# Optimization experiments

Measured on AMD Instinct MI355X. Metric: run time of the kernel, lower is better.

## Reference

```python
import jax, jax.numpy as jnp
import numpy as np

HEADS = 16
DIMS = [64, 64, 64, 64]  # [d_att(Q), d_att(K), d_ff(V), d_ff(G)]
EPS = 1e-4
P_POW = 2


def _cdist(Q, K):
    # Euclidean pairwise distance via the norm expansion, like torch.cdist.
    # Q: [h, b, t, d], K: [h, b, t, d] -> [h, b, t, t]
    q2 = jnp.sum(Q * Q, axis=-1)  # [h, b, t]
    k2 = jnp.sum(K * K, axis=-1)  # [h, b, t]
    qk = jnp.einsum('hbtd,hbsd->hbts', Q, K)
    d2 = q2[..., :, None] + k2[..., None, :] - 2.0 * qk
    return jnp.sqrt(jnp.maximum(d2, 0.0))


def setup_inputs() -> dict:
    key = jax.random.key(0)
    ks = jax.random.split(key, 4)
    b, t, d_in = 2, 2048, 1024
    d_proj = HEADS * sum(DIMS)  # 4096
    X = jax.random.normal(ks[0], (b, t, d_in), dtype=jnp.float32)
    W_in = jax.random.normal(ks[1], (d_in, d_proj), dtype=jnp.float32) * (d_in ** -0.5)
    b_in = jnp.zeros((d_proj,), dtype=jnp.float32)
    W_out = jax.random.normal(ks[2], (HEADS * DIMS[2], d_in), dtype=jnp.float32) * ((HEADS * DIMS[2]) ** -0.5)
    b_out = jnp.zeros((d_in,), dtype=jnp.float32)
    return {"X": X, "W_in": W_in, "b_in": b_in, "W_out": W_out, "b_out": b_out}


def reference(X, W_in, b_in, W_out, b_out):
    b, t, _ = X.shape
    # multi-head input projection: [b,t,d_in] -> [h,b,t,sum(DIMS)] -> split
    P = X @ W_in + b_in                       # [b, t, h*sum(DIMS)]
    P = P.reshape(b, t, HEADS, sum(DIMS))
    P = jnp.transpose(P, (2, 0, 1, 3))        # [h, b, t, sum(DIMS)]
    splits = np.cumsum(DIMS)[:-1]
    Q, K, V, G = jnp.split(P, splits, axis=-1)
    # Shepard's attention: inverse-power-distance weights
    W = jnp.power(EPS + _cdist(Q, K), -P_POW)         # [h, b, t, t]
    W = W / (EPS + jnp.sum(W, axis=-1, keepdims=True))
    A = jnp.einsum('hbts,hbse->hbte', W, V)           # [h, b, t, e]
    H = G * A                                          # gating
    H = jnp.transpose(H, (1, 2, 0, 3)).reshape(b, t, HEADS * DIMS[2])
    return H @ W_out + b_out
```

## Files before the change

kernel.cpp:

```cpp
#include <hip/hip_runtime.h>
#include <hip/hip_bf16.h>
#include <cstdint>
#include <cstddef>

typedef __bf16 bf16_t;
typedef __attribute__((ext_vector_type(8))) __bf16 bf16x8;
typedef __attribute__((ext_vector_type(4))) float f32x4;
typedef __attribute__((ext_vector_type(16))) float f32x16;
typedef __attribute__((ext_vector_type(4))) unsigned int u32x4;

#define ATT_EPS 1e-4f

__device__ __forceinline__ f32x4 mfma_bf16(bf16x8 a, bf16x8 b, f32x4 c) {
  return __builtin_amdgcn_mfma_f32_16x16x32_bf16(a, b, c, 0, 0, 0);
}
__device__ __forceinline__ f32x16 mfma32(bf16x8 a, bf16x8 b, f32x16 c) {
  return __builtin_amdgcn_mfma_f32_32x32x16_bf16(a, b, c, 0, 0, 0);
}
__device__ __forceinline__ unsigned cvtpk_bf16(float lo, float hi) {
  unsigned r;
  asm("v_cvt_pk_bf16_f32 %0, %1, %2" : "=v"(r) : "v"(lo), "v"(hi));
  return r;
}

#define GLDS16(g, l)                                                          \
  __builtin_amdgcn_global_load_lds(                                           \
      (const __attribute__((address_space(1))) void*)(g),                     \
      (__attribute__((address_space(3))) void*)(l), 16, 0, 0)

__global__ __launch_bounds__(256) void cvt_x_kernel(
    const float* __restrict__ X, bf16_t* __restrict__ Xb, int n8) {
  int i = blockIdx.x * 256 + threadIdx.x;
  if (i >= n8) return;
  f32x4 a = ((const f32x4*)X)[i * 2 + 0];
  f32x4 b = ((const f32x4*)X)[i * 2 + 1];
  bf16x8 o;
  o[0] = (__bf16)a[0]; o[1] = (__bf16)a[1]; o[2] = (__bf16)a[2]; o[3] = (__bf16)a[3];
  o[4] = (__bf16)b[0]; o[5] = (__bf16)b[1]; o[6] = (__bf16)b[2]; o[7] = (__bf16)b[3];
  ((bf16x8*)Xb)[i] = o;
}

__global__ __launch_bounds__(256) void tcvt2_kernel(
    const float* __restrict__ Wi, bf16_t* __restrict__ WiT,
    const float* __restrict__ Wo, bf16_t* __restrict__ WoT) {
  __shared__ float T[64][65];
  int tx = threadIdx.x & 63, ty = threadIdx.x >> 6;
  const float* W;
  bf16_t* Wt;
  int c0, r0, R, C;
  if (blockIdx.y < 16) {
    W = Wi; Wt = WiT; R = 1024; C = 4096;
    c0 = blockIdx.x * 64; r0 = blockIdx.y * 64;
  } else {
    int idx = (blockIdx.y - 16) * 64 + blockIdx.x;
    if (idx >= 256) return;
    W = Wo; Wt = WoT; R = 1024; C = 1024;
    c0 = (idx & 15) * 64; r0 = (idx >> 4) * 64;
  }
#pragma unroll
  for (int i = 0; i < 16; ++i) {
    int rr = ty * 16 + i;
    T[rr][tx] = W[(size_t)(r0 + rr) * C + c0 + tx];
  }
  __syncthreads();
#pragma unroll
  for (int i = 0; i < 16; ++i) {
    int cc = ty * 16 + i;
    Wt[(size_t)(c0 + cc) * R + r0 + tx] = (bf16_t)T[tx][cc];
  }
}

template <int OUTF32, int FUSE>
__global__ __launch_bounds__(256, 2) void gemm_kernel(
    const bf16_t* __restrict__ A, const bf16_t* __restrict__ Bt,
    const float* __restrict__ bias, void* __restrict__ Cout,
    int M, int N, int K,
    float* __restrict__ Q2, bf16_t* __restrict__ K2E, bf16_t* __restrict__ VtG) {
  __shared__ bf16_t As[2][128 * 64];
  __shared__ bf16_t Bs[2][128 * 64];
  int tid = threadIdx.x, lane = tid & 63, wv = tid >> 6;
  int l15 = lane & 15, lhi = lane >> 4;
  int NT = N >> 7;
  int nwg = gridDim.x;
  int qq = nwg >> 3;
  int swz = (blockIdx.x & 7) * qq + (blockIdx.x >> 3);
  int tm = swz / NT, tn = swz % NT;
  int m0 = tm << 7, n0 = tn << 7;
  int wm = (wv >> 1) << 6, wn = (wv & 1) << 6;
  int KT = K >> 6;

  auto stage = [&](int buf, int kt) {
    int k0 = kt << 6;
#pragma unroll
    for (int s = 0; s < 4; ++s) {
      int t = s * 256 + tid;
      int row = t >> 3, u = t & 7;
      int cc = (u ^ (row & 7)) << 3;
      GLDS16(A + (size_t)(m0 + row) * K + k0 + cc, &As[buf][t * 8]);
    }
#pragma unroll
    for (int s = 0; s < 4; ++s) {
      int t = s * 256 + tid;
      int row = t >> 3, u = t & 7;
      int cc = (u ^ (row & 7)) << 3;
      GLDS16(Bt + (size_t)(n0 + row) * K + k0 + cc, &Bs[buf][t * 8]);
    }
  };

  f32x4 zero = {0.f, 0.f, 0.f, 0.f};
  f32x4 acc[4][4];
#pragma unroll
  for (int ms = 0; ms < 4; ++ms)
#pragma unroll
    for (int ns = 0; ns < 4; ++ns) acc[ms][ns] = zero;

  stage(0, 0);
  __syncthreads();
  int cur = 0;
  for (int kt = 0; kt < KT; ++kt) {
    if (kt + 1 < KT) stage(cur ^ 1, kt + 1);
#pragma unroll
    for (int ks = 0; ks < 2; ++ks) {
      bf16x8 af[4], bfr[4];
#pragma unroll
      for (int ms = 0; ms < 4; ++ms) {
        int row = wm + ms * 16 + l15;
        af[ms] = *(const bf16x8*)&As[cur][row * 64 + (((ks * 4 + lhi) ^ (row & 7)) << 3)];
      }
#pragma unroll
      for (int ns = 0; ns < 4; ++ns) {
        int col = wn + ns * 16 + l15;
        bfr[ns] = *(const bf16x8*)&Bs[cur][col * 64 + (((ks * 4 + lhi) ^ (col & 7)) << 3)];
      }
#pragma unroll
      for (int ms = 0; ms < 4; ++ms)
#pragma unroll
        for (int ns = 0; ns < 4; ++ns)
          acc[ms][ns] = mfma_bf16(af[ms], bfr[ns], acc[ms][ns]);
    }
    __syncthreads();
    cur ^= 1;
  }

#pragma unroll
  for (int ns = 0; ns < 4; ++ns) {
    float bv = bias[n0 + wn + ns * 16 + l15];
#pragma unroll
    for (int ms = 0; ms < 4; ++ms)
#pragma unroll
      for (int r = 0; r < 4; ++r) acc[ms][ns][r] += bv;
  }

  bool vg = FUSE && ((n0 >> 7) & 1);
  bool skipC = vg && (wn == 0);

  if (!skipC) {
#pragma unroll
    for (int ns = 0; ns < 4; ++ns) {
      int col = n0 + wn + ns * 16 + l15;
#pragma unroll
      for (int ms = 0; ms < 4; ++ms) {
        int rowb = m0 + wm + ms * 16 + lhi * 4;
#pragma unroll
        for (int r = 0; r < 4; ++r) {
          float v = acc[ms][ns][r];
          if (OUTF32)
            ((float*)Cout)[(size_t)(rowb + r) * N + col] = v;
          else
            ((bf16_t*)Cout)[(size_t)(rowb + r) * N + col] = (bf16_t)v;
        }
      }
    }
  }

  if (FUSE) {
    int h = n0 >> 8;
    if (!vg) {
#pragma unroll
      for (int ms = 0; ms < 4; ++ms)
#pragma unroll
        for (int r = 0; r < 4; ++r) {
          float s = 0.f;
#pragma unroll
          for (int ns = 0; ns < 4; ++ns) s += acc[ms][ns][r] * acc[ms][ns][r];
          s += __shfl_xor(s, 1);
          s += __shfl_xor(s, 2);
          s += __shfl_xor(s, 4);
          s += __shfl_xor(s, 8);
          if (l15 == 0) {
            int row = m0 + wm + ms * 16 + lhi * 4 + r;
            if (wn == 0) {
              Q2[h * 4096 + row] = s;
            } else {
              __bf16 kh = (__bf16)s;
              __bf16 kl = (__bf16)(s - (float)kh);
              bf16x8 rw;
              rw[0] = kh; rw[1] = kl;
              rw[2] = (__bf16)1.f; rw[3] = (__bf16)1.f;
              rw[4] = (__bf16)0.f; rw[5] = (__bf16)0.f;
              rw[6] = (__bf16)0.f; rw[7] = (__bf16)0.f;
              *(bf16x8*)&K2E[((size_t)h * 4096 + row) * 8] = rw;
            }
          }
        }
    } else {
      bf16_t* T = (bf16_t*)&As[0][0];
      if (wn == 0) {
#pragma unroll
        for (int ms = 0; ms < 4; ++ms)
#pragma unroll
          for (int ns = 0; ns < 4; ++ns)
#pragma unroll
            for (int r = 0; r < 4; ++r) {
              int row = wm + ms * 16 + lhi * 4 + r;
              int e = ns * 16 + l15;
              int prow = (row & ~15) | ((row & 3) | ((row & 4) << 1) | ((row & 8) >> 1));
              T[e * 136 + prow] = (bf16_t)acc[ms][ns][r];
            }
      }
      __syncthreads();
      int e = tid >> 2, c0 = (tid & 3) * 32;
      bf16_t* dst = VtG + (size_t)(h * 64 + e) * 4096 + m0 + c0;
#pragma unroll
      for (int j = 0; j < 4; ++j)
        *(bf16x8*)&dst[j * 8] = *(bf16x8*)&T[e * 136 + c0 + j * 8];
    }
  }
}

__global__ __launch_bounds__(512, 4) void attn_kernel(
    const bf16_t* __restrict__ P, const bf16_t* __restrict__ VtG,
    const float* __restrict__ Q2, const bf16_t* __restrict__ K2E,
    bf16_t* __restrict__ H) {
  __shared__ union Smem {
    struct {
      bf16_t Ks[2][64 * 64];
      bf16_t Vts[2][64 * 64];
      bf16_t K2e[2][64 * 8];
    } l;
    float Comb[4][64][33];
  } sm;
  __shared__ float invLds[4][32];

  int tid = threadIdx.x, lane = tid & 63, wv = tid >> 6;
  int l31 = lane & 31, hi = lane >> 5, hi4 = hi * 4;
  int qw = wv & 3, sw = wv >> 2;
  int sOff = sw * 32;
  int swz = (blockIdx.x & 7) * 64 + (blockIdx.x >> 3);
  int hb = swz >> 4, qt = swz & 15;
  int h = hb >> 1, b = hb & 1;
  int rowbase = b * 2048;
  const bf16_t* Pq = P + (size_t)rowbase * 4096 + h * 256;
  const bf16_t* Pk = Pq + 64;
  const bf16_t* Pg = Pq + 192;
  const bf16_t* Vg = VtG + (size_t)h * 64 * 4096 + rowbase;
  const float* Q2g = Q2 + h * 4096 + rowbase;
  const bf16_t* K2Eg = K2E + ((size_t)h * 4096 + rowbase) * 8;
  int q0 = qt * 128 + qw * 32;

  auto stageKV = [&](int buf, int s0) {
    {
      int row = tid >> 3, u = tid & 7;
      int cc = (u ^ (row & 7)) << 3;
      GLDS16(Pk + (size_t)(s0 + row) * 4096 + cc, &sm.l.Ks[buf][tid * 8]);
    }
    {
      int row = tid >> 3, u = tid & 7;
      int cc = (u ^ (row & 7)) << 3;
      GLDS16(Vg + (size_t)row * 4096 + s0 + cc, &sm.l.Vts[buf][tid * 8]);
    }
    if (tid < 64)
      GLDS16(K2Eg + (size_t)(s0 + tid) * 8, &sm.l.K2e[buf][tid * 8]);
  };

  bf16x8 qm[4];
#pragma unroll
  for (int db = 0; db < 4; ++db) {
    bf16x8 q = *(const bf16x8*)(Pq + (size_t)(q0 + l31) * 4096 + db * 16 + hi * 8);
    u32x4 u = *(u32x4*)&q;
    u = (u ^ 0x80008000u) + 0x00800080u;
    qm[db] = *(bf16x8*)&u;
  }
  float q2s = Q2g[q0 + l31];
  __bf16 q2h = (__bf16)q2s;
  __bf16 q2l = (__bf16)(q2s - (float)q2h);
  bf16x8 qmE;
  qmE[0] = hi ? (__bf16)0.f : (__bf16)1.f;
  qmE[1] = qmE[0];
  qmE[2] = hi ? (__bf16)0.f : q2h;
  qmE[3] = hi ? (__bf16)0.f : q2l;
  qmE[4] = (__bf16)0.f; qmE[5] = (__bf16)0.f;
  qmE[6] = (__bf16)0.f; qmE[7] = (__bf16)0.f;

  f32x16 zero16;
#pragma unroll
  for (int r = 0; r < 16; ++r) zero16[r] = 0.f;

  f32x16 nacc0 = zero16, nacc1 = zero16;
  float dacc0 = 0.f, dacc1 = 0.f;

  stageKV(0, 0);
  __syncthreads();

  for (int st = 0; st < 32; ++st) {
    int cur = st & 1;
    int s0 = st * 64;
    if (st + 1 < 32) stageKV(cur ^ 1, s0 + 64);

    const bf16_t* KsC = sm.l.Ks[cur];
    const bf16_t* VtC = sm.l.Vts[cur];
    const bf16_t* K2eC = sm.l.K2e[cur];
    {
      int srow = sOff + l31;
      bf16x8 ke = *(const bf16x8*)&K2eC[srow * 8];
      u32x4 keu = *(u32x4*)&ke;
      u32x4 kz;
      kz[0] = hi ? 0u : keu[0];
      kz[1] = hi ? 0u : keu[1];
      kz[2] = 0u; kz[3] = 0u;
      bf16x8 kfE = *(bf16x8*)&kz;
      f32x16 D = mfma32(kfE, qmE, zero16);
#pragma unroll
      for (int db = 0; db < 4; ++db) {
        bf16x8 kf = *(const bf16x8*)&KsC[srow * 64 + (((db * 2 + hi) ^ (srow & 7)) << 3)];
        D = mfma32(kf, qm[db], D);
      }
      float p[16];
#pragma unroll
      for (int r = 0; r < 16; ++r) {
        float w = __builtin_amdgcn_rcpf(fmaxf(D[r], 1e-12f));
        if (r & 1) dacc1 += w; else dacc0 += w;
        p[r] = w;
      }
      u32x4 w0v = {cvtpk_bf16(p[0], p[1]), cvtpk_bf16(p[2], p[3]),
                   cvtpk_bf16(p[4], p[5]), cvtpk_bf16(p[6], p[7])};
      u32x4 w1v = {cvtpk_bf16(p[8], p[9]), cvtpk_bf16(p[10], p[11]),
                   cvtpk_bf16(p[12], p[13]), cvtpk_bf16(p[14], p[15])};
      bf16x8 pa0 = *(bf16x8*)&w0v;
      bf16x8 pa1 = *(bf16x8*)&w1v;
      int e = l31;
      int ciB = sw * 4;
      bf16x8 vb00 = *(const bf16x8*)&VtC[e * 64 + (((ciB + 0 + hi) ^ (e & 7)) << 3)];
      bf16x8 vb01 = *(const bf16x8*)&VtC[(e + 32) * 64 + (((ciB + 0 + hi) ^ ((e + 32) & 7)) << 3)];
      bf16x8 vb10 = *(const bf16x8*)&VtC[e * 64 + (((ciB + 2 + hi) ^ (e & 7)) << 3)];
      bf16x8 vb11 = *(const bf16x8*)&VtC[(e + 32) * 64 + (((ciB + 2 + hi) ^ ((e + 32) & 7)) << 3)];
      nacc0 = mfma32(pa0, vb00, nacc0);
      nacc1 = mfma32(pa0, vb01, nacc1);
      nacc0 = mfma32(pa1, vb10, nacc0);
      nacc1 = mfma32(pa1, vb11, nacc1);
    }
    __syncthreads();
  }

  if (sw == 1) {
#pragma unroll
    for (int r = 0; r < 16; ++r) {
      sm.Comb[qw][lane][r] = nacc0[r];
      sm.Comb[qw][lane][16 + r] = nacc1[r];
    }
    sm.Comb[qw][lane][32] = dacc0 + dacc1;
  }
  __syncthreads();
  if (sw == 0) {
    float dacc = dacc0 + dacc1 + sm.Comb[qw][lane][32];
#pragma unroll
    for (int r = 0; r < 16; ++r) {
      nacc0[r] += sm.Comb[qw][lane][r];
      nacc1[r] += sm.Comb[qw][lane][16 + r];
    }
    dacc += __shfl_xor(dacc, 32);
    float inv = __builtin_amdgcn_rcpf(ATT_EPS + dacc);
    if (lane < 32) invLds[qw][l31] = inv;
    __builtin_amdgcn_s_waitcnt(0);
#pragma unroll
    for (int r = 0; r < 16; ++r) {
      int q = (r & 3) + 8 * (r >> 2) + hi4;
      int tq = q0 + q;
      float iv = invLds[qw][q];
      float g0 = (float)Pg[(size_t)tq * 4096 + l31];
      float g1 = (float)Pg[(size_t)tq * 4096 + 32 + l31];
      H[(size_t)(rowbase + tq) * 1024 + h * 64 + l31] = (bf16_t)(g0 * nacc0[r] * iv);
      H[(size_t)(rowbase + tq) * 1024 + h * 64 + 32 + l31] = (bf16_t)(g1 * nacc1[r] * iv);
    }
  }
}

extern "C" void kernel_launch(void* const* d_in, const int* in_sizes, int n_in,
                              void* d_out, int out_size, void* d_ws, size_t ws_size,
                              hipStream_t stream) {
  const float* X     = (const float*)d_in[0];
  const float* W_in  = (const float*)d_in[1];
  const float* b_in  = (const float*)d_in[2];
  const float* W_out = (const float*)d_in[3];
  const float* b_out = (const float*)d_in[4];

  char* ws = (char*)d_ws;
  bf16_t* Xb  = (bf16_t*)(ws);
  bf16_t* WbT = (bf16_t*)(ws + ((size_t)8  << 20));
  bf16_t* WoT = (bf16_t*)(ws + ((size_t)16 << 20));
  bf16_t* Pb  = (bf16_t*)(ws + ((size_t)18 << 20));
  bf16_t* Hb  = (bf16_t*)(ws + ((size_t)50 << 20));
  float*  Q2  = (float*) (ws + ((size_t)58 << 20));
  bf16_t* VtG = (bf16_t*)d_out;
  bf16_t* K2E = (bf16_t*)((char*)d_out + ((size_t)8 << 20));

  cvt_x_kernel<<<2048, 256, 0, stream>>>(X, Xb, 4096 * 1024 / 8);
  tcvt2_kernel<<<dim3(64, 20), 256, 0, stream>>>(W_in, WbT, W_out, WoT);
  gemm_kernel<0, 1><<<1024, 256, 0, stream>>>(Xb, WbT, b_in, Pb, 4096, 4096, 1024,
                                              Q2, K2E, VtG);
  attn_kernel<<<512, 512, 0, stream>>>(Pb, VtG, Q2, K2E, Hb);
  gemm_kernel<1, 0><<<256, 256, 0, stream>>>(Hb, WoT, b_out, d_out, 4096, 1024, 1024,
                                             nullptr, nullptr, nullptr);
}
```

Measured before the change: 131.8 us.

## Add dedicated 256x256-tile input projection GEMM with 4-stage direct-to-LDS pipeline

Replaces the generic 128x128-tile GEMM used for the input projection with a specialized kernel. It uses 512 threads, 256x256 output tiles (one head per tile), K-step 32 and a 4-buffer LDS ring filled by direct global-to-LDS loads (GLDS16), with MFMAs interleaved between the staging phases. The larger tile raises arithmetic intensity and cuts the number of workgroups. The fused Q/K norm and V-transpose epilogue is adapted to the new tile shape. Risks are lower occupancy with only 256 workgroups and heavier register use from 32 accumulators per thread.

```diff
diff --git a/kernel.cpp b/kernel.cpp
--- a/kernel.cpp
+++ b/kernel.cpp
@@ -70,12 +70,172 @@
   }
 }
 
-template <int OUTF32, int FUSE>
+__global__ __launch_bounds__(512, 2) void gemm1_kernel(
+    const bf16_t* __restrict__ A, const bf16_t* __restrict__ Bt,
+    const float* __restrict__ bias, bf16_t* __restrict__ P,
+    float* __restrict__ Q2, bf16_t* __restrict__ K2E, bf16_t* __restrict__ VtG) {
+  __shared__ bf16_t As[4][2][128 * 32];
+  __shared__ bf16_t Bs[4][2][128 * 32];
+
+  const int K = 1024, N = 4096;
+  int tid = threadIdx.x, lane = tid & 63, wv = tid >> 6;
+  int l15 = lane & 15, lhi = lane >> 4;
+  int wm = wv >> 2, wn = wv & 3;
+  int swz = (blockIdx.x & 7) * 32 + (blockIdx.x >> 3);
+  int tm = swz >> 4, tn = swz & 15;
+  int m0 = tm << 8, n0 = tn << 8;
+  int h = tn;
+
+  int srow = tid >> 2, su = tid & 3;
+  int scc = (su ^ ((srow >> 1) & 3)) << 3;
+  auto stage2 = [&](int t, int pq) {
+    int k0 = t * 32 + scc;
+    if (pq == 0) {
+      GLDS16(A + (size_t)(m0 + srow) * K + k0, &As[t & 3][0][tid * 8]);
+      GLDS16(A + (size_t)(m0 + 128 + srow) * K + k0, &As[t & 3][1][tid * 8]);
+    } else {
+      GLDS16(Bt + (size_t)(n0 + srow) * K + k0, &Bs[t & 3][0][tid * 8]);
+      GLDS16(Bt + (size_t)(n0 + 128 + srow) * K + k0, &Bs[t & 3][1][tid * 8]);
+    }
+  };
+
+  f32x4 zero = {0.f, 0.f, 0.f, 0.f};
+  f32x4 acc[8][4];
+#pragma unroll
+  for (int mf = 0; mf < 8; ++mf)
+#pragma unroll
+    for (int nf = 0; nf < 4; ++nf) acc[mf][nf] = zero;
+
+  int bh = wn >> 1;
+  int cidb = (wn & 1) * 64 + l15;
+
+  stage2(0, 0); stage2(0, 1);
+  stage2(1, 0); stage2(1, 1);
+  asm volatile("s_waitcnt vmcnt(4)" ::: "memory");
+  __syncthreads();
+
+  for (int t = 0; t < 32; ++t) {
+    int buf = t & 3;
+    bf16x8 af0[4], bfr[4];
+#pragma unroll
+    for (int i = 0; i < 4; ++i) {
+      int mfr = i * 16 + l15;
+      af0[i] = *(const bf16x8*)&As[buf][wm][mfr * 32 + ((lhi ^ ((mfr >> 1) & 3)) << 3)];
+    }
+#pragma unroll
+    for (int nf = 0; nf < 4; ++nf) {
+      int cid = cidb + nf * 16;
+      bfr[nf] = *(const bf16x8*)&Bs[buf][bh][cid * 32 + ((lhi ^ ((cid >> 1) & 3)) << 3)];
+    }
+    if (t + 2 < 32) stage2(t + 2, 0);
+    __syncthreads();
+#pragma unroll
+    for (int i = 0; i < 4; ++i)
+#pragma unroll
+      for (int nf = 0; nf < 4; ++nf)
+        acc[i][nf] = mfma_bf16(af0[i], bfr[nf], acc[i][nf]);
+    bf16x8 af1[4];
+#pragma unroll
+    for (int i = 0; i < 4; ++i) {
+      int mfr = (4 + i) * 16 + l15;
+      af1[i] = *(const bf16x8*)&As[buf][wm][mfr * 32 + ((lhi ^ ((mfr >> 1) & 3)) << 3)];
+    }
+    if (t + 2 < 32) stage2(t + 2, 1);
+    if (t < 30) {
+      asm volatile("s_waitcnt vmcnt(4)" ::: "memory");
+    } else if (t == 30) {
+      asm volatile("s_waitcnt vmcnt(0)" ::: "memory");
+    }
+    __syncthreads();
+#pragma unroll
+    for (int i = 0; i < 4; ++i)
+#pragma unroll
+      for (int nf = 0; nf < 4; ++nf)
+        acc[4 + i][nf] = mfma_bf16(af1[i], bfr[nf], acc[4 + i][nf]);
+  }
+
+#pragma unroll
+  for (int nf = 0; nf < 4; ++nf) {
+    float bv = bias[n0 + wn * 64 + nf * 16 + l15];
+#pragma unroll
+    for (int mf = 0; mf < 8; ++mf)
+#pragma unroll
+      for (int r = 0; r < 4; ++r) acc[mf][nf][r] += bv;
+  }
+
+  if (wn != 2) {
+#pragma unroll
+    for (int nf = 0; nf < 4; ++nf) {
+      int col = n0 + wn * 64 + nf * 16 + l15;
+#pragma unroll
+      for (int mf = 0; mf < 8; ++mf) {
+        int rowb = m0 + wm * 128 + mf * 16 + lhi * 4;
+#pragma unroll
+        for (int r = 0; r < 4; ++r)
+          P[(size_t)(rowb + r) * N + col] = (bf16_t)acc[mf][nf][r];
+      }
+    }
+  }
+
+  if (wn < 2) {
+#pragma unroll
+    for (int mf = 0; mf < 8; ++mf)
+#pragma unroll
+      for (int r = 0; r < 4; ++r) {
+        float s = 0.f;
+#pragma unroll
+        for (int nf = 0; nf < 4; ++nf) s += acc[mf][nf][r] * acc[mf][nf][r];
+        s += __shfl_xor(s, 1);
+        s += __shfl_xor(s, 2);
+        s += __shfl_xor(s, 4);
+        s += __shfl_xor(s, 8);
+        if (l15 == 0) {
+          int row = m0 + wm * 128 + mf * 16 + lhi * 4 + r;
+          if (wn == 0) {
+            Q2[h * 4096 + row] = s;
+          } else {
+            __bf16 kh = (__bf16)s;
+            __bf16 kl = (__bf16)(s - (float)kh);
+            bf16x8 rw;
+            rw[0] = kh; rw[1] = kl;
+            rw[2] = (__bf16)1.f; rw[3] = (__bf16)1.f;
+            rw[4] = (__bf16)0.f; rw[5] = (__bf16)0.f;
+            rw[6] = (__bf16)0.f; rw[7] = (__bf16)0.f;
+            *(bf16x8*)&K2E[((size_t)h * 4096 + row) * 8] = rw;
+          }
+        }
+      }
+  }
+
+  bf16_t* T = &As[0][0][0];
+  if (wn == 2) {
+#pragma unroll
+    for (int mf = 0; mf < 8; ++mf)
+#pragma unroll
+      for (int nf = 0; nf < 4; ++nf)
+#pragma unroll
+        for (int r = 0; r < 4; ++r) {
+          int row = wm * 128 + mf * 16 + lhi * 4 + r;
+          int e = nf * 16 + l15;
+          int prow = (row & ~15) | ((row & 3) | ((row & 4) << 1) | ((row & 8) >> 1));
+          T[e * 264 + prow] = (bf16_t)acc[mf][nf][r];
+        }
+  }
+  __syncthreads();
+  {
+    int e = tid >> 3, c0 = (tid & 7) * 32;
+    bf16_t* dst = VtG + (size_t)(h * 64 + e) * 4096 + m0 + c0;
+#pragma unroll
+    for (int j = 0; j < 4; ++j)
+      *(bf16x8*)&dst[j * 8] = *(bf16x8*)&T[e * 264 + c0 + j * 8];
+  }
+}
+
+template <int OUTF32>
 __global__ __launch_bounds__(256, 2) void gemm_kernel(
     const bf16_t* __restrict__ A, const bf16_t* __restrict__ Bt,
     const float* __restrict__ bias, void* __restrict__ Cout,
-    int M, int N, int K,
-    float* __restrict__ Q2, bf16_t* __restrict__ K2E, bf16_t* __restrict__ VtG) {
+    int M, int N, int K) {
   __shared__ bf16_t As[2][128 * 64];
   __shared__ bf16_t Bs[2][128 * 64];
   int tid = threadIdx.x, lane = tid & 63, wv = tid >> 6;
@@ -144,86 +304,19 @@
 
 #pragma unroll
   for (int ns = 0; ns < 4; ++ns) {
-    float bv = bias[n0 + wn + ns * 16 + l15];
-#pragma unroll
-    for (int ms = 0; ms < 4; ++ms)
-#pragma unroll
-      for (int r = 0; r < 4; ++r) acc[ms][ns][r] += bv;
-  }
-
-  bool vg = FUSE && ((n0 >> 7) & 1);
-  bool skipC = vg && (wn == 0);
-
-  if (!skipC) {
-#pragma unroll
-    for (int ns = 0; ns < 4; ++ns) {
-      int col = n0 + wn + ns * 16 + l15;
-#pragma unroll
-      for (int ms = 0; ms < 4; ++ms) {
-        int rowb = m0 + wm + ms * 16 + lhi * 4;
-#pragma unroll
-        for (int r = 0; r < 4; ++r) {
-          float v = acc[ms][ns][r];
-          if (OUTF32)
-            ((float*)Cout)[(size_t)(rowb + r) * N + col] = v;
-          else
-            ((bf16_t*)Cout)[(size_t)(rowb + r) * N + col] = (bf16_t)v;
-        }
-      }
-    }
-  }
-
-  if (FUSE) {
-    int h = n0 >> 8;
-    if (!vg) {
-#pragma unroll
-      for (int ms = 0; ms < 4; ++ms)
-#pragma unroll
-        for (int r = 0; r < 4; ++r) {
-          float s = 0.f;
-#pragma unroll
-          for (int ns = 0; ns < 4; ++ns) s += acc[ms][ns][r] * acc[ms][ns][r];
-          s += __shfl_xor(s, 1);
-          s += __shfl_xor(s, 2);
-          s += __shfl_xor(s, 4);
-          s += __shfl_xor(s, 8);
-          if (l15 == 0) {
-            int row = m0 + wm + ms * 16 + lhi * 4 + r;
-            if (wn == 0) {
-              Q2[h * 4096 + row] = s;
-            } else {
-              __bf16 kh = (__bf16)s;
-              __bf16 kl = (__bf16)(s - (float)kh);
-              bf16x8 rw;
-              rw[0] = kh; rw[1] = kl;
-              rw[2] = (__bf16)1.f; rw[3] = (__bf16)1.f;
-              rw[4] = (__bf16)0.f; rw[5] = (__bf16)0.f;
-              rw[6] = (__bf16)0.f; rw[7] = (__bf16)0.f;
-              *(bf16x8*)&K2E[((size_t)h * 4096 + row) * 8] = rw;
-            }
-          }
-        }
-    } else {
-      bf16_t* T = (bf16_t*)&As[0][0];
-      if (wn == 0) {
-#pragma unroll
-        for (int ms = 0; ms < 4; ++ms)
-#pragma unroll
-          for (int ns = 0; ns < 4; ++ns)
-#pragma unroll
-            for (int r = 0; r < 4; ++r) {
-              int row = wm + ms * 16 + lhi * 4 + r;
-              int e = ns * 16 + l15;
-              int prow = (row & ~15) | ((row & 3) | ((row & 4) << 1) | ((row & 8) >> 1));
-              T[e * 136 + prow] = (bf16_t)acc[ms][ns][r];
-            }
-      }
-      __syncthreads();
-      int e = tid >> 2, c0 = (tid & 3) * 32;
-      bf16_t* dst = VtG + (size_t)(h * 64 + e) * 4096 + m0 + c0;
-#pragma unroll
-      for (int j = 0; j < 4; ++j)
-        *(bf16x8*)&dst[j * 8] = *(bf16x8*)&T[e * 136 + c0 + j * 8];
+    int col = n0 + wn + ns * 16 + l15;
+    float bv = bias[col];
+#pragma unroll
+    for (int ms = 0; ms < 4; ++ms) {
+      int rowb = m0 + wm + ms * 16 + lhi * 4;
+#pragma unroll
+      for (int r = 0; r < 4; ++r) {
+        float v = acc[ms][ns][r] + bv;
+        if (OUTF32)
+          ((float*)Cout)[(size_t)(rowb + r) * N + col] = v;
+        else
+          ((bf16_t*)Cout)[(size_t)(rowb + r) * N + col] = (bf16_t)v;
+      }
     }
   }
 }
@@ -406,9 +499,7 @@
 
   cvt_x_kernel<<<2048, 256, 0, stream>>>(X, Xb, 4096 * 1024 / 8);
   tcvt2_kernel<<<dim3(64, 20), 256, 0, stream>>>(W_in, WbT, W_out, WoT);
-  gemm_kernel<0, 1><<<1024, 256, 0, stream>>>(Xb, WbT, b_in, Pb, 4096, 4096, 1024,
-                                              Q2, K2E, VtG);
+  gemm1_kernel<<<256, 512, 0, stream>>>(Xb, WbT, b_in, Pb, Q2, K2E, VtG);
   attn_kernel<<<512, 512, 0, stream>>>(Pb, VtG, Q2, K2E, Hb);
-  gemm_kernel<1, 0><<<256, 256, 0, stream>>>(Hb, WoT, b_out, d_out, 4096, 1024, 1024,
-                                             nullptr, nullptr, nullptr);
-}
+  gemm_kernel<1><<<256, 256, 0, stream>>>(Hb, WoT, b_out, d_out, 4096, 1024, 1024);
+}
```

New measurement: 140.9 us. 1.07x slower.
